# Kernel optimization log

Hardware: AMD Instinct MI355X
Metric: run time of the kernel (lower is better)

The kernel has to match this reference:

```python
import jax, jax.numpy as jnp
import numpy as np

BASIS_SIZE = 256          # levels of the bitfield code
R_MAX = 1.0               # quantization range for normalized weights
QMAX = BASIS_SIZE // 2 - 1  # 127 -> symmetric int8-style grid
EPS = 1e-8


def setup_inputs() -> dict:
    key = jax.random.key(0)
    kx, kw, kb = jax.random.split(key, 3)
    B, S, D_IN, D_OUT = 4, 2048, 4096, 4096
    x = jax.random.normal(kx, (B, S, D_IN), dtype=jnp.float32)
    W = jax.random.normal(kw, (D_OUT, D_IN), dtype=jnp.float32)
    bias = jax.random.normal(kb, (D_OUT,), dtype=jnp.float32)
    return {"x": x, "W": W, "bias": bias}


def _bitfield_dequant_weight(W):
    # per-output-row L2 norm (p=2, dim=1 in torch)
    weight_norms = jnp.sqrt(jnp.sum(W * W, axis=1))          # [out]
    W_normalized = W / (weight_norms[:, None] + EPS)          # rows ~unit norm
    # bitfield encode/decode: uniform symmetric quantization to BASIS_SIZE
    # levels in [-R_MAX, R_MAX]
    scale = R_MAX / QMAX
    Wq = jnp.round(jnp.clip(W_normalized, -R_MAX, R_MAX) / scale) * scale
    return Wq, weight_norms


def reference(x, W, bias):
    Wq, weight_norms = _bitfield_dequant_weight(W)
    B, S, D_IN = x.shape
    x2 = x.reshape(-1, D_IN)                                  # [B*S, in]
    # bitfield matmul on normalized weights
    out_norm = jnp.einsum('nd,od->no', x2, Wq)                # [B*S, out]
    # denormalize (restore row norms) + bias epilogue
    out = out_norm * weight_norms
    out = out.reshape(B, S, -1) + bias
    return out
```

## Files before the change

### kernel.cpp

```cpp
#include <hip/hip_runtime.h>
#include <hip/hip_bf16.h>

typedef __attribute__((ext_vector_type(4))) int i32x4;

#define D_IN  4096
#define D_OUT 4096
#define M_TOT 8192

__device__ __forceinline__ void async16(const void* g, void* l) {
  __builtin_amdgcn_global_load_lds(
      (__attribute__((address_space(1))) void*)g,
      (__attribute__((address_space(3))) void*)l,
      16, 0, 0);
}

__device__ __forceinline__ int pack4(float a, float b, float c, float d, float s) {
  int q0 = (int)rintf(a * s) & 255;
  int q1 = (int)rintf(b * s) & 255;
  int q2 = (int)rintf(c * s) & 255;
  int q3 = (int)rintf(d * s) & 255;
  return q0 | (q1 << 8) | (q2 << 16) | (q3 << 24);
}

__global__ void quant_x_kernel(const float* __restrict__ x, int4* __restrict__ xq,
                               float* __restrict__ sx) {
  const int row = blockIdx.x;
  const int t = threadIdx.x;
  const float* xr = x + (size_t)row * D_IN;

  float4 v[4];
  float mx = 0.f;
#pragma unroll
  for (int j = 0; j < 4; j++) {
    v[j] = ((const float4*)xr)[t * 4 + j];
    mx = fmaxf(mx, fmaxf(fmaxf(fabsf(v[j].x), fabsf(v[j].y)),
                         fmaxf(fabsf(v[j].z), fabsf(v[j].w))));
  }
#pragma unroll
  for (int off = 32; off; off >>= 1) mx = fmaxf(mx, __shfl_down(mx, off));
  __shared__ float red[4];
  __shared__ float smx;
  if ((t & 63) == 0) red[t >> 6] = mx;
  __syncthreads();
  if (t == 0) {
    float m = fmaxf(fmaxf(red[0], red[1]), fmaxf(red[2], red[3]));
    smx = m;
    sx[row] = m * (1.0f / 127.0f);
  }
  __syncthreads();

  const float inv = 127.0f / smx;
  int4 o;
  o.x = pack4(v[0].x, v[0].y, v[0].z, v[0].w, inv);
  o.y = pack4(v[1].x, v[1].y, v[1].z, v[1].w, inv);
  o.z = pack4(v[2].x, v[2].y, v[2].z, v[2].w, inv);
  o.w = pack4(v[3].x, v[3].y, v[3].z, v[3].w, inv);
  xq[(size_t)row * (D_IN / 16) + t] = o;
}

__global__ void quant_w_kernel(const float* __restrict__ W, int4* __restrict__ wq,
                               float* __restrict__ sn) {
  const int row = blockIdx.x;
  const int t = threadIdx.x;
  const float* wr = W + (size_t)row * D_IN;

  float4 v[4];
  double ss = 0.0;
#pragma unroll
  for (int j = 0; j < 4; j++) {
    v[j] = ((const float4*)wr)[t * 4 + j];
    ss += (double)v[j].x * v[j].x + (double)v[j].y * v[j].y +
          (double)v[j].z * v[j].z + (double)v[j].w * v[j].w;
  }
#pragma unroll
  for (int off = 32; off; off >>= 1) ss += __shfl_down(ss, off);
  __shared__ double red[4];
  __shared__ float shn;
  if ((t & 63) == 0) red[t >> 6] = ss;
  __syncthreads();
  if (t == 0) {
    double tot = red[0] + red[1] + red[2] + red[3];
    float nrm = (float)sqrt(tot);
    shn = nrm;
    sn[row] = nrm * (1.0f / 127.0f);
  }
  __syncthreads();

  const float den = shn + 1e-8f;
  int4 o;
  int* op = (int*)&o;
#pragma unroll
  for (int j = 0; j < 4; j++) {
    float e[4] = {v[j].x, v[j].y, v[j].z, v[j].w};
    int q[4];
#pragma unroll
    for (int c = 0; c < 4; c++) {
      float wn = e[c] / den;
      wn = fminf(1.0f, fmaxf(-1.0f, wn));
      q[c] = (int)rintf(wn * 127.0f) & 255;
    }
    op[j] = q[0] | (q[1] << 8) | (q[2] << 16) | (q[3] << 24);
  }
  wq[(size_t)row * (D_IN / 16) + t] = o;
}

__global__ void gemm_i8_kernel(const char* __restrict__ A, const char* __restrict__ B,
                               const float* __restrict__ sx, const float* __restrict__ sn,
                               const float* __restrict__ bias, float* __restrict__ C) {
  __shared__ __align__(16) char lds_a[128 * 64];
  __shared__ __align__(16) char lds_b[128 * 64];

  const int t = threadIdx.x;
  const int lane = t & 63;
  const int wave = t >> 6;
  const int wm = wave >> 1, wn = wave & 1;
  const int m0 = blockIdx.y * 128;
  const int n0 = blockIdx.x * 128;

  const int srow = t >> 2;
  const int skc = (t & 3) ^ (srow & 3);
  const char* gA = A + (size_t)(m0 + srow) * D_IN + skc * 16;
  const char* gB = B + (size_t)(n0 + srow) * D_IN + skc * 16;
  char* lA = lds_a + t * 16;
  char* lB = lds_b + t * 16;
  const size_t rstride = (size_t)64 * D_IN;

  const int ml = lane & 15;
  const int g = lane >> 4;
  const int xorb = (g ^ (ml & 3)) * 16;
  const char* ra = lds_a + (wm * 64 + ml) * 64 + xorb;
  const char* rb = lds_b + (wn * 64 + ml) * 64 + xorb;

  i32x4 acc[4][4];
#pragma unroll
  for (int i = 0; i < 4; i++)
#pragma unroll
    for (int j = 0; j < 4; j++) acc[i][j] = (i32x4)0;

  for (int k0 = 0; k0 < D_IN; k0 += 64) {
    async16(gA, lA);
    async16(gA + rstride, lA + 4096);
    async16(gB, lB);
    async16(gB + rstride, lB + 4096);
    gA += 64; gB += 64;
    __syncthreads();

    i32x4 af[4], bfr[4];
#pragma unroll
    for (int i = 0; i < 4; i++) {
      af[i]  = *(const i32x4*)(ra + i * 16 * 64);
      bfr[i] = *(const i32x4*)(rb + i * 16 * 64);
    }
#pragma unroll
    for (int mi = 0; mi < 4; mi++)
#pragma unroll
      for (int ni = 0; ni < 4; ni++)
        acc[mi][ni] = __builtin_amdgcn_mfma_i32_16x16x64_i8(af[mi], bfr[ni], acc[mi][ni], 0, 0, 0);
    __syncthreads();
  }

  float scn[4], bsv[4];
#pragma unroll
  for (int ni = 0; ni < 4; ni++) {
    const int col = n0 + wn * 64 + ni * 16 + ml;
    scn[ni] = sn[col];
    bsv[ni] = bias[col];
  }
#pragma unroll
  for (int mi = 0; mi < 4; mi++) {
    const int rbase = m0 + wm * 64 + mi * 16 + g * 4;
    float sxv[4];
#pragma unroll
    for (int r = 0; r < 4; r++) sxv[r] = sx[rbase + r];
#pragma unroll
    for (int ni = 0; ni < 4; ni++) {
      const int col = n0 + wn * 64 + ni * 16 + ml;
#pragma unroll
      for (int r = 0; r < 4; r++)
        C[(size_t)(rbase + r) * D_OUT + col] =
            (float)acc[mi][ni][r] * (sxv[r] * scn[ni]) + bsv[ni];
    }
  }
}

extern "C" void kernel_launch(void* const* d_in, const int* in_sizes, int n_in,
                              void* d_out, int out_size, void* d_ws, size_t ws_size,
                              hipStream_t stream) {
  const float* x    = (const float*)d_in[0];
  const float* W    = (const float*)d_in[1];
  const float* bias = (const float*)d_in[2];
  float* out = (float*)d_out;

  char* ws = (char*)d_ws;
  char*  xq = ws;
  char*  wq = ws + (size_t)M_TOT * D_IN;
  float* sx = (float*)(wq + (size_t)D_OUT * D_IN);
  float* sn = sx + M_TOT;

  quant_x_kernel<<<M_TOT, 256, 0, stream>>>(x, (int4*)xq, sx);
  quant_w_kernel<<<D_OUT, 256, 0, stream>>>(W, (int4*)wq, sn);
  dim3 grid(D_OUT / 128, M_TOT / 128);
  gemm_i8_kernel<<<grid, 256, 0, stream>>>(xq, wq, sx, sn, bias, out);
}
```

Measured before the change: 420.3 us.

## Triple-buffer LDS in int8 GEMM with async prefetch and inline-asm reads

```diff
diff --git a/kernel.cpp b/kernel.cpp
--- a/kernel.cpp
+++ b/kernel.cpp
@@ -2,17 +2,22 @@
 #include <hip/hip_bf16.h>
 
 typedef __attribute__((ext_vector_type(4))) int i32x4;
+typedef __attribute__((address_space(3))) char lds3;
 
 #define D_IN  4096
 #define D_OUT 4096
 #define M_TOT 8192
-
-__device__ __forceinline__ void async16(const void* g, void* l) {
+#define RSTRIDE ((size_t)64 * D_IN)
+
+__device__ __forceinline__ void async16(const void* g, lds3* l) {
   __builtin_amdgcn_global_load_lds(
       (__attribute__((address_space(1))) void*)g,
       (__attribute__((address_space(3))) void*)l,
       16, 0, 0);
 }
+
+#define DSR(dst, addr, off) \
+  asm volatile("ds_read_b128 %0, %1 offset:%2" : "=v"(dst) : "v"(addr), "i"(off))
 
 __device__ __forceinline__ int pack4(float a, float b, float c, float d, float s) {
   int q0 = (int)rintf(a * s) & 255;
@@ -104,11 +109,43 @@
   wq[(size_t)row * (D_IN / 16) + t] = o;
 }
 
-__global__ void gemm_i8_kernel(const char* __restrict__ A, const char* __restrict__ B,
-                               const float* __restrict__ sx, const float* __restrict__ sn,
-                               const float* __restrict__ bias, float* __restrict__ C) {
-  __shared__ __align__(16) char lds_a[128 * 64];
-  __shared__ __align__(16) char lds_b[128 * 64];
+template<int S, int VM, bool ISSUE>
+__device__ __forceinline__ void k_iter(unsigned aA, unsigned aB,
+                                       const char* pA, const char* pB,
+                                       lds3* lA, lds3* lB,
+                                       i32x4 (&acc)[4][4]) {
+  asm volatile("s_waitcnt vmcnt(%0)" :: "i"(VM));
+  asm volatile("s_barrier" ::: "memory");
+  if (ISSUE) {
+    async16(pA, lA);
+    async16(pA + RSTRIDE, lA + 4096);
+    async16(pB, lB);
+    async16(pB + RSTRIDE, lB + 4096);
+  }
+  i32x4 af[4], bf[4];
+  DSR(af[0], aA, S * 16384 + 0);
+  DSR(af[1], aA, S * 16384 + 1024);
+  DSR(af[2], aA, S * 16384 + 2048);
+  DSR(af[3], aA, S * 16384 + 3072);
+  DSR(bf[0], aB, S * 16384 + 8192 + 0);
+  DSR(bf[1], aB, S * 16384 + 8192 + 1024);
+  DSR(bf[2], aB, S * 16384 + 8192 + 2048);
+  DSR(bf[3], aB, S * 16384 + 8192 + 3072);
+  asm volatile("s_waitcnt lgkmcnt(0)"
+               : "+v"(af[0]), "+v"(af[1]), "+v"(af[2]), "+v"(af[3]),
+                 "+v"(bf[0]), "+v"(bf[1]), "+v"(bf[2]), "+v"(bf[3]));
+#pragma unroll
+  for (int mi = 0; mi < 4; mi++)
+#pragma unroll
+    for (int ni = 0; ni < 4; ni++)
+      acc[mi][ni] = __builtin_amdgcn_mfma_i32_16x16x64_i8(af[mi], bf[ni], acc[mi][ni], 0, 0, 0);
+}
+
+__global__ __launch_bounds__(256, 3)
+void gemm_i8_kernel(const char* __restrict__ A, const char* __restrict__ B,
+                    const float* __restrict__ sx, const float* __restrict__ sn,
+                    const float* __restrict__ bias, float* __restrict__ C) {
+  __shared__ __align__(16) char smem[3 * 16384];
 
   const int t = threadIdx.x;
   const int lane = t & 63;
@@ -118,18 +155,20 @@
   const int n0 = blockIdx.x * 128;
 
   const int srow = t >> 2;
-  const int skc = (t & 3) ^ (srow & 3);
-  const char* gA = A + (size_t)(m0 + srow) * D_IN + skc * 16;
-  const char* gB = B + (size_t)(n0 + srow) * D_IN + skc * 16;
-  char* lA = lds_a + t * 16;
-  char* lB = lds_b + t * 16;
-  const size_t rstride = (size_t)64 * D_IN;
+  const int q = ((t & 3) - ((srow & 15) >> 1)) & 3;
+  const char* gA = A + (size_t)(m0 + srow) * D_IN + q * 16;
+  const char* gB = B + (size_t)(n0 + srow) * D_IN + q * 16;
+
+  lds3* l3 = (lds3*)smem;
+  lds3* lA0 = l3 + t * 16;
+  lds3* lB0 = l3 + 8192 + t * 16;
 
   const int ml = lane & 15;
   const int g = lane >> 4;
-  const int xorb = (g ^ (ml & 3)) * 16;
-  const char* ra = lds_a + (wm * 64 + ml) * 64 + xorb;
-  const char* rb = lds_b + (wn * 64 + ml) * 64 + xorb;
+  const unsigned cperm = (unsigned)((g + (ml >> 1)) & 3);
+  const unsigned lds_base = (unsigned)(size_t)l3;
+  const unsigned aA = lds_base + (wm * 64 + ml) * 64 + cperm * 16;
+  const unsigned aB = lds_base + (wn * 64 + ml) * 64 + cperm * 16;
 
   i32x4 acc[4][4];
 #pragma unroll
@@ -137,27 +176,24 @@
 #pragma unroll
     for (int j = 0; j < 4; j++) acc[i][j] = (i32x4)0;
 
-  for (int k0 = 0; k0 < D_IN; k0 += 64) {
-    async16(gA, lA);
-    async16(gA + rstride, lA + 4096);
-    async16(gB, lB);
-    async16(gB + rstride, lB + 4096);
-    gA += 64; gB += 64;
-    __syncthreads();
-
-    i32x4 af[4], bfr[4];
-#pragma unroll
-    for (int i = 0; i < 4; i++) {
-      af[i]  = *(const i32x4*)(ra + i * 16 * 64);
-      bfr[i] = *(const i32x4*)(rb + i * 16 * 64);
-    }
-#pragma unroll
-    for (int mi = 0; mi < 4; mi++)
-#pragma unroll
-      for (int ni = 0; ni < 4; ni++)
-        acc[mi][ni] = __builtin_amdgcn_mfma_i32_16x16x64_i8(af[mi], bfr[ni], acc[mi][ni], 0, 0, 0);
-    __syncthreads();
-  }
+  async16(gA, lA0);            async16(gA + RSTRIDE, lA0 + 4096);
+  async16(gB, lB0);            async16(gB + RSTRIDE, lB0 + 4096);
+  async16(gA + 64, lA0 + 16384);           async16(gA + 64 + RSTRIDE, lA0 + 16384 + 4096);
+  async16(gB + 64, lB0 + 16384);           async16(gB + 64 + RSTRIDE, lB0 + 16384 + 4096);
+
+  const char* pA = gA + 128;
+  const char* pB = gB + 128;
+
+#pragma unroll 1
+  for (int tr = 0; tr < 20; ++tr) {
+    k_iter<0, 4, true>(aA, aB, pA, pB, lA0 + 32768, lB0 + 32768, acc); pA += 64; pB += 64;
+    k_iter<1, 4, true>(aA, aB, pA, pB, lA0,         lB0,         acc); pA += 64; pB += 64;
+    k_iter<2, 4, true>(aA, aB, pA, pB, lA0 + 16384, lB0 + 16384, acc); pA += 64; pB += 64;
+  }
+  k_iter<0, 4, true >(aA, aB, pA, pB, lA0 + 32768, lB0 + 32768, acc); pA += 64; pB += 64;
+  k_iter<1, 4, true >(aA, aB, pA, pB, lA0,         lB0,         acc);
+  k_iter<2, 4, false>(aA, aB, pA, pB, lA0,         lB0,         acc);
+  k_iter<0, 0, false>(aA, aB, pA, pB, lA0,         lB0,         acc);
 
   float scn[4], bsv[4];
 #pragma unroll
```

After: 405.4 us. -3.6%, faster.
